# Kernel optimization log

Hardware: AMD Instinct MI355X
Metric: run time of the kernel (lower is better)

## Reference

```python
import jax, jax.numpy as jnp
import numpy as np

N, E, D_IN, D, HEADS = 8192, 2048, 256, 256, 4
EPS = 1e-5
NEG = -1e9  # large negative instead of -inf (rows guaranteed non-empty anyway)


def _layernorm(x, g, b):
    mu = jnp.mean(x, axis=-1, keepdims=True)
    var = jnp.mean(jnp.square(x - mu), axis=-1, keepdims=True)
    return (x - mu) * jax.lax.rsqrt(var + EPS) * g + b


def _mha(q_x, kv_x, in_w, in_b, out_w, out_b, mask):
    """torch nn.MultiheadAttention (batch=1, eval) with boolean attn_mask.
    q_x: [Lq, D], kv_x: [Lk, D], mask: [Lq, Lk] True = blocked."""
    hd = D // HEADS
    wq, wk, wv = jnp.split(in_w, 3, axis=0)   # each [D, D]
    bq, bk, bv = jnp.split(in_b, 3, axis=0)
    q = (q_x @ wq.T + bq).reshape(-1, HEADS, hd).transpose(1, 0, 2)  # [h, Lq, hd]
    k = (kv_x @ wk.T + bk).reshape(-1, HEADS, hd).transpose(1, 0, 2)
    v = (kv_x @ wv.T + bv).reshape(-1, HEADS, hd).transpose(1, 0, 2)
    scores = jnp.einsum('hqd,hkd->hqk', q, k) / jnp.sqrt(jnp.asarray(hd, q.dtype))
    scores = jnp.where(mask[None, :, :], NEG, scores)
    attn = jax.nn.softmax(scores, axis=-1)
    out = jnp.einsum('hqk,hkd->hqd', attn, v)           # [h, Lq, hd]
    out = out.transpose(1, 0, 2).reshape(-1, D)          # [Lq, D]
    return out @ out_w.T + out_b


def setup_inputs() -> dict:
    key = jax.random.key(0)
    ks = jax.random.split(key, 12)
    s = 0.02
    x_0 = jax.random.normal(ks[0], (N, D_IN), jnp.float32)
    x_1 = jax.random.normal(ks[1], (E, D_IN), jnp.float32)
    H = (jax.random.uniform(ks[2], (N, E)) < 0.01).astype(jnp.float32)
    H = H.at[jnp.arange(N), jnp.arange(N) % E].set(1.0)
    return {
        'x_0': x_0, 'x_1': x_1, 'incidence_1': H,
        'node_w': jax.random.normal(ks[3], (D, D_IN), jnp.float32) * s,
        'node_b': jnp.zeros((D,), jnp.float32),
        'edge_w': jax.random.normal(ks[4], (D, D_IN), jnp.float32) * s,
        'edge_b': jnp.zeros((D,), jnp.float32),
        'n2e_in_w': jax.random.normal(ks[5], (3 * D, D), jnp.float32) * s,
        'n2e_in_b': jnp.zeros((3 * D,), jnp.float32),
        'n2e_out_w': jax.random.normal(ks[6], (D, D), jnp.float32) * s,
        'n2e_out_b': jnp.zeros((D,), jnp.float32),
        'e2n_in_w': jax.random.normal(ks[7], (3 * D, D), jnp.float32) * s,
        'e2n_in_b': jnp.zeros((3 * D,), jnp.float32),
        'e2n_out_w': jax.random.normal(ks[8], (D, D), jnp.float32) * s,
        'e2n_out_b': jnp.zeros((D,), jnp.float32),
        'norm1_g': jnp.ones((D,), jnp.float32),
        'norm1_b': jnp.zeros((D,), jnp.float32),
        'norm2_g': jnp.ones((D,), jnp.float32),
        'norm2_b': jnp.zeros((D,), jnp.float32),
    }


def reference(x_0, x_1, incidence_1, node_w, node_b, edge_w, edge_b,
              n2e_in_w, n2e_in_b, n2e_out_w, n2e_out_b,
              e2n_in_w, e2n_in_b, e2n_out_w, e2n_out_b,
              norm1_g, norm1_b, norm2_g, norm2_b):
    H = incidence_1                      # [N, E]
    x_0_p = x_0 @ node_w.T + node_b      # [N, D]
    x_1_p = x_1 @ edge_w.T + edge_b      # [E, D]
    # node -> edge: edges query nodes, mask where H.T == 0
    x_1_u = _mha(x_1_p, x_0_p, n2e_in_w, n2e_in_b, n2e_out_w, n2e_out_b,
                 H.T == 0)
    x_1_u = _layernorm(x_1_p + x_1_u, norm1_g, norm1_b)
    # edge -> node: nodes query updated edges, mask where H == 0
    x_0_u = _mha(x_0_p, x_1_u, e2n_in_w, e2n_in_b, e2n_out_w, e2n_out_b,
                 H == 0)
    x_0_u = _layernorm(x_0_p + x_0_u, norm2_g, norm2_b)
    return (x_0_u, x_1_u)
```

## Files before the change

kernel.cpp:

```cpp
#include <hip/hip_runtime.h>
#include <hip/hip_bf16.h>

using bf16 = __hip_bfloat16;
typedef __attribute__((ext_vector_type(4))) float  f32x4;
typedef __attribute__((ext_vector_type(8))) short  s16x8;

#define QSTRIDE 1040
#define CMAX 256
#define RMAX 128

struct ConvDesc { const float* src[12]; int dstoff[12]; int cnt[12]; };

__global__ __launch_bounds__(256)
void conv_weights(ConvDesc d, bf16* __restrict__ dst)
{
    const int seg = blockIdx.x >> 6;
    const int blk = blockIdx.x & 63;
    const float* __restrict__ s = d.src[seg];
    bf16* __restrict__ o = dst + d.dstoff[seg];
    const int n = d.cnt[seg];
    for (int i = blk * 256 + threadIdx.x; i < n; i += 64 * 256)
        o[i] = __float2bfloat16(s[i]);
}

__global__ __launch_bounds__(256)
void build_lists(const float* __restrict__ H, int* __restrict__ col_cnt,
                 unsigned short* __restrict__ col_idx, int* __restrict__ row_cnt,
                 unsigned short* __restrict__ row_idx)
{
    const int n = blockIdx.x, t = threadIdx.x;
    __shared__ int rc;
    if (t == 0) rc = 0;
    __syncthreads();

    const float* Hp = H + (size_t)n * 2048 + t * 8;
    f32x4 h0 = *(const f32x4*)Hp;
    f32x4 h1 = *(const f32x4*)(Hp + 4);
    float hv[8];
#pragma unroll
    for (int j = 0; j < 4; j++) { hv[j] = h0[j]; hv[4 + j] = h1[j]; }

#pragma unroll
    for (int j = 0; j < 8; j++) {
        if (hv[j] != 0.f) {
            const int e = t * 8 + j;
            const int sr = atomicAdd(&rc, 1);
            if (sr < RMAX) row_idx[(size_t)n * RMAX + sr] = (unsigned short)e;
            const int sc = atomicAdd(&col_cnt[e], 1);
            if (sc < CMAX) col_idx[(size_t)e * CMAX + sc] = (unsigned short)n;
        }
    }
    __syncthreads();
    if (t == 0) row_cnt[n] = (rc < RMAX) ? rc : RMAX;
}

template<bool AF32>
__global__ __launch_bounds__(256, 2)
void gemm_bt(const void* __restrict__ Av, const bf16* __restrict__ W,
             const bf16* __restrict__ bias, bf16* __restrict__ outB,
             int K, int N, int tilesN)
{
    __shared__ __align__(16) bf16 As[4 * QSTRIDE];
    __shared__ __align__(16) bf16 Bs[4 * QSTRIDE];

    const int t    = threadIdx.x;
    const int lane = t & 63;
    const int w    = t >> 6;
    const int wm   = (w >> 1) * 64;
    const int wn   = (w & 1) * 64;
    const int tm   = (blockIdx.x / tilesN) * 128;
    const int tn   = (blockIdx.x % tilesN) * 128;

    f32x4 acc[4][4];
#pragma unroll
    for (int i = 0; i < 4; i++)
#pragma unroll
        for (int j = 0; j < 4; j++)
#pragma unroll
            for (int r = 0; r < 4; r++) acc[i][j][r] = 0.f;

    const int m0 = t >> 2,         q0 = t & 3;
    const int m1 = (t + 256) >> 2, q1 = (t + 256) & 3;

    const int fq = lane >> 4;
    const int fr = lane & 15;

    for (int k0 = 0; k0 < K; k0 += 32) {
        s16x8 sa0, sa1;
        if (AF32) {
            const float* Af = (const float*)Av;
            f32x4 a0l = *(const f32x4*)(Af + (size_t)(tm + m0) * K + k0 + q0 * 8);
            f32x4 a0h = *(const f32x4*)(Af + (size_t)(tm + m0) * K + k0 + q0 * 8 + 4);
            f32x4 a1l = *(const f32x4*)(Af + (size_t)(tm + m1) * K + k0 + q1 * 8);
            f32x4 a1h = *(const f32x4*)(Af + (size_t)(tm + m1) * K + k0 + q1 * 8 + 4);
            union { s16x8 v; bf16 e[8]; } u0, u1;
#pragma unroll
            for (int j = 0; j < 4; j++) {
                u0.e[j] = __float2bfloat16(a0l[j]); u0.e[4 + j] = __float2bfloat16(a0h[j]);
                u1.e[j] = __float2bfloat16(a1l[j]); u1.e[4 + j] = __float2bfloat16(a1h[j]);
            }
            sa0 = u0.v; sa1 = u1.v;
        } else {
            const bf16* Ab = (const bf16*)Av;
            sa0 = *(const s16x8*)(Ab + (size_t)(tm + m0) * K + k0 + q0 * 8);
            sa1 = *(const s16x8*)(Ab + (size_t)(tm + m1) * K + k0 + q1 * 8);
        }
        s16x8 sb0 = *(const s16x8*)(W + (size_t)(tn + m0) * K + k0 + q0 * 8);
        s16x8 sb1 = *(const s16x8*)(W + (size_t)(tn + m1) * K + k0 + q1 * 8);

        __syncthreads();
        *(s16x8*)&As[q0 * QSTRIDE + m0 * 8] = sa0;
        *(s16x8*)&As[q1 * QSTRIDE + m1 * 8] = sa1;
        *(s16x8*)&Bs[q0 * QSTRIDE + m0 * 8] = sb0;
        *(s16x8*)&Bs[q1 * QSTRIDE + m1 * 8] = sb1;
        __syncthreads();

        s16x8 af[4], bfv[4];
#pragma unroll
        for (int i = 0; i < 4; i++) {
            af[i]  = *(const s16x8*)&As[fq * QSTRIDE + (wm + i * 16 + fr) * 8];
            bfv[i] = *(const s16x8*)&Bs[fq * QSTRIDE + (wn + i * 16 + fr) * 8];
        }
#pragma unroll
        for (int i = 0; i < 4; i++)
#pragma unroll
            for (int j = 0; j < 4; j++)
                acc[i][j] = __builtin_amdgcn_mfma_f32_16x16x32_bf16(
                    af[i], bfv[j], acc[i][j], 0, 0, 0);
    }

#pragma unroll
    for (int j = 0; j < 4; j++) {
        const int ncol = tn + wn + j * 16 + fr;
        const float bj = __bfloat162float(bias[ncol]);
#pragma unroll
        for (int i = 0; i < 4; i++)
#pragma unroll
            for (int r = 0; r < 4; r++) {
                const int mrow = tm + wm + i * 16 + fq * 4 + r;
                outB[(size_t)mrow * N + ncol] = __float2bfloat16(acc[i][j][r] + bj);
            }
    }
}

__global__ __launch_bounds__(256)
void sparse_attn(const bf16* __restrict__ Q, const bf16* __restrict__ Kb,
                 const bf16* __restrict__ Vb, int kvs,
                 const int* __restrict__ cnts, const unsigned short* __restrict__ idx,
                 int lmax, int idxmask, bf16* __restrict__ out)
{
    __shared__ float sc[4][CMAX];
    __shared__ unsigned short nls[CMAX];
    const int qi   = blockIdx.x;
    const int h    = threadIdx.x >> 6;
    const int lane = threadIdx.x & 63;
    const int grp  = lane >> 3;
    const int sub  = lane & 7;

    int n = cnts[qi];
    if (n > lmax) n = lmax;

    if (h == 0)
        for (int i = lane; i < n; i += 64)
            nls[i] = (unsigned short)(((int)idx[(size_t)qi * lmax + i]) & idxmask);
    __syncthreads();

    if (n <= 0) {
        out[(size_t)qi * 256 + h * 64 + lane] = __float2bfloat16(0.f);
        return;
    }

    float qv[8];
    {
        union { f32x4 v; unsigned short u[8]; } qu;
        qu.v = *(const f32x4*)(Q + (size_t)qi * 256 + h * 64 + sub * 8);
#pragma unroll
        for (int j = 0; j < 8; j++)
            qv[j] = __uint_as_float(((unsigned)qu.u[j]) << 16) * 0.125f;
    }

    float mx = -1e30f;
#pragma unroll 2
    for (int base = 0; base < n; base += 8) {
        const int i = base + grp;
        float s = -1e30f;
        if (i < n) {
            const int nb = nls[i];
            union { f32x4 v; unsigned short u[8]; } ku;
            ku.v = *(const f32x4*)(Kb + (size_t)nb * kvs + h * 64 + sub * 8);
            float a = 0.f;
#pragma unroll
            for (int j = 0; j < 8; j++)
                a += __uint_as_float(((unsigned)ku.u[j]) << 16) * qv[j];
            a += __shfl_xor(a, 1);
            a += __shfl_xor(a, 2);
            a += __shfl_xor(a, 4);
            if (sub == 0) sc[h][i] = a;
            s = a;
        }
        mx = fmaxf(mx, s);
    }
#pragma unroll
    for (int o = 32; o > 0; o >>= 1) mx = fmaxf(mx, __shfl_xor(mx, o));

    float sum = 0.f;
    for (int base = 0; base < n; base += 64) {
        const int i = base + lane;
        if (i < n) {
            const float p = __expf(sc[h][i] - mx);
            sc[h][i] = p;
            sum += p;
        }
    }
#pragma unroll
    for (int o = 32; o > 0; o >>= 1) sum += __shfl_xor(sum, o);
    const float inv = 1.f / sum;

    float oa[8];
#pragma unroll
    for (int j = 0; j < 8; j++) oa[j] = 0.f;
#pragma unroll 2
    for (int base = 0; base < n; base += 8) {
        const int i = base + grp;
        if (i < n) {
            const float p = sc[h][i];
            const int nb = nls[i];
            union { f32x4 v; unsigned short u[8]; } vu;
            vu.v = *(const f32x4*)(Vb + (size_t)nb * kvs + h * 64 + sub * 8);
#pragma unroll
            for (int j = 0; j < 8; j++)
                oa[j] += p * __uint_as_float(((unsigned)vu.u[j]) << 16);
        }
    }
#pragma unroll
    for (int j = 0; j < 8; j++) {
        oa[j] += __shfl_xor(oa[j], 8);
        oa[j] += __shfl_xor(oa[j], 16);
        oa[j] += __shfl_xor(oa[j], 32);
    }
    if (grp == 0) {
        union { s16x8 v; bf16 e[8]; } ou;
#pragma unroll
        for (int j = 0; j < 8; j++) ou.e[j] = __float2bfloat16(oa[j] * inv);
        *(s16x8*)(out + (size_t)qi * 256 + h * 64 + sub * 8) = ou.v;
    }
}

__global__ __launch_bounds__(256)
void residual_ln(const bf16* __restrict__ xp, const bf16* __restrict__ mh,
                 const float* __restrict__ g, const float* __restrict__ b,
                 float* __restrict__ outF, bf16* __restrict__ outB)
{
    const int row = blockIdx.x, t = threadIdx.x;
    __shared__ float red1[4], red2[4];
    const float x = __bfloat162float(xp[(size_t)row * 256 + t])
                  + __bfloat162float(mh[(size_t)row * 256 + t]);

    float s = x;
#pragma unroll
    for (int o = 32; o > 0; o >>= 1) s += __shfl_xor(s, o);
    if ((t & 63) == 0) red1[t >> 6] = s;
    __syncthreads();
    const float mu = (red1[0] + red1[1] + red1[2] + red1[3]) * (1.f / 256.f);

    const float d = x - mu;
    float v = d * d;
#pragma unroll
    for (int o = 32; o > 0; o >>= 1) v += __shfl_xor(v, o);
    if ((t & 63) == 0) red2[t >> 6] = v;
    __syncthreads();
    const float var = (red2[0] + red2[1] + red2[2] + red2[3]) * (1.f / 256.f);

    const float y = d * rsqrtf(var + 1e-5f) * g[t] + b[t];
    outF[(size_t)row * 256 + t] = y;
    if (outB) outB[(size_t)row * 256 + t] = __float2bfloat16(y);
}

extern "C" void kernel_launch(void* const* d_in, const int* in_sizes, int n_in,
                              void* d_out, int out_size, void* d_ws, size_t ws_size,
                              hipStream_t stream)
{
    const int N = 8192, E = 2048;

    float* out0 = (float*)d_out;
    float* out1 = (float*)d_out + (size_t)N * 256;

    char* wp = (char*)d_ws;
    auto carve = [&](size_t bytes) { void* p = wp; wp += (bytes + 15) & ~size_t(15); return p; };

    bf16*  wcat    = (bf16*)          carve(657920 * 2);
    int*   col_cnt = (int*)           carve((size_t)E * 4);
    int*   row_cnt = (int*)           carve((size_t)N * 4);
    unsigned short* col_idx = (unsigned short*)carve((size_t)E * CMAX * 2);
    unsigned short* row_idx = (unsigned short*)carve((size_t)N * RMAX * 2);
    bf16*  x0p     = (bf16*)          carve((size_t)N * 256 * 2);
    bf16*  x1p     = (bf16*)          carve((size_t)E * 256 * 2);
    bf16*  x1u_b   = (bf16*)          carve((size_t)E * 256 * 2);
    bf16*  R1      = (bf16*)          carve((size_t)N * 512 * 2);
    bf16*  R2      = (bf16*)          carve((size_t)E * 256 * 3 * 2);

    bf16* kv1   = R1;
    bf16* q2    = R1;
    bf16* attn2 = R1 + (size_t)N * 256;
    bf16* mha2  = R1;
    bf16* q1    = R2;
    bf16* attn1 = R2 + (size_t)E * 256;
    bf16* mha1  = R2 + (size_t)E * 512;
    bf16* kv2   = R2;

    const int O_NW = 0, O_EW = 65536, O_AIW = 131072, O_AOW = 327680,
              O_BIW = 393216, O_BOW = 589824, O_NB = 655360, O_EB = 655616,
              O_AIB = 655872, O_AOB = 656640, O_BIB = 656896, O_BOB = 657664;

    ConvDesc cd;
    const int srcix[12] = {3, 5, 7, 9, 11, 13, 4, 6, 8, 10, 12, 14};
    const int offs [12] = {O_NW, O_EW, O_AIW, O_AOW, O_BIW, O_BOW,
                           O_NB, O_EB, O_AIB, O_AOB, O_BIB, O_BOB};
    const int cnts [12] = {65536, 65536, 196608, 65536, 196608, 65536,
                           256, 256, 768, 256, 768, 256};
    for (int i = 0; i < 12; i++) {
        cd.src[i] = (const float*)d_in[srcix[i]];
        cd.dstoff[i] = offs[i];
        cd.cnt[i] = cnts[i];
    }
    conv_weights<<<12 * 64, 256, 0, stream>>>(cd, wcat);

    hipMemsetAsync(col_cnt, 0, (size_t)E * 4, stream);
    build_lists<<<N, 256, 0, stream>>>((const float*)d_in[2], col_cnt, col_idx,
                                       row_cnt, row_idx);

    gemm_bt<true><<<(N/128)*2, 256, 0, stream>>>(d_in[0], wcat + O_NW,
                                                 wcat + O_NB, x0p, 256, 256, 2);
    gemm_bt<true><<<(E/128)*2, 256, 0, stream>>>(d_in[1], wcat + O_EW,
                                                 wcat + O_EB, x1p, 256, 256, 2);

    gemm_bt<false><<<(E/128)*2, 256, 0, stream>>>(x1p, wcat + O_AIW,
                                                  wcat + O_AIB, q1, 256, 256, 2);
    gemm_bt<false><<<(N/128)*4, 256, 0, stream>>>(x0p, wcat + O_AIW + 65536,
                                                  wcat + O_AIB + 256, kv1, 256, 512, 4);
    sparse_attn<<<E, 256, 0, stream>>>(q1, kv1, kv1 + 256, 512,
                                       col_cnt, col_idx, CMAX, N - 1, attn1);
    gemm_bt<false><<<(E/128)*2, 256, 0, stream>>>(attn1, wcat + O_AOW,
                                                  wcat + O_AOB, mha1, 256, 256, 2);
    residual_ln<<<E, 256, 0, stream>>>(x1p, mha1, (const float*)d_in[15],
                                       (const float*)d_in[16], out1, x1u_b);

    gemm_bt<false><<<(N/128)*2, 256, 0, stream>>>(x0p, wcat + O_BIW,
                                                  wcat + O_BIB, q2, 256, 256, 2);
    gemm_bt<false><<<(E/128)*4, 256, 0, stream>>>(x1u_b, wcat + O_BIW + 65536,
                                                  wcat + O_BIB + 256, kv2, 256, 512, 4);
    sparse_attn<<<N, 256, 0, stream>>>(q2, kv2, kv2 + 256, 512,
                                       row_cnt, row_idx, RMAX, E - 1, attn2);
    gemm_bt<false><<<(N/128)*2, 256, 0, stream>>>(attn2, wcat + O_BOW,
                                                  wcat + O_BOB, mha2, 256, 256, 2);
    residual_ln<<<N, 256, 0, stream>>>(x0p, mha2, (const float*)d_in[17],
                                       (const float*)d_in[18], out0, nullptr);
}
```

Measured before the change: 288.1 us.

## Merge projection GEMMs, batch KV/Q GEMMs, fuse out-proj with residual LayerNorm

The two input projections become one launch (gemm_proj), which handles both the node and edge fp32 inputs. The node-side K/V projection for attention 1 and the Q projection for attention 2 are merged into a single 768-wide GEMM. The separate residual_ln kernels are removed: a new gemm_ln computes the output projection over full 256-column rows, adds bias and residual, and applies LayerNorm in the epilogue using shared-memory row reductions. This cuts kernel launches and intermediate round-trips through global memory. In exchange, gemm_ln uses 64-row tiles (fewer blocks) and computes variance as E[x^2]-mu^2, which can be less precise.

```diff
diff --git a/kernel.cpp b/kernel.cpp
--- a/kernel.cpp
+++ b/kernel.cpp
@@ -6,10 +6,12 @@
 typedef __attribute__((ext_vector_type(8))) short  s16x8;
 
 #define QSTRIDE 1040
+#define ASTRIDE 520
+#define BSTRIDE 2064
 #define CMAX 256
 #define RMAX 128
 
-struct ConvDesc { const float* src[12]; int dstoff[12]; int cnt[12]; };
+struct ConvDesc { const float* src[14]; int dstoff[14]; int cnt[14]; };
 
 __global__ __launch_bounds__(256)
 void conv_weights(ConvDesc d, bf16* __restrict__ dst)
@@ -54,9 +56,8 @@
     if (t == 0) row_cnt[n] = (rc < RMAX) ? rc : RMAX;
 }
 
-template<bool AF32>
 __global__ __launch_bounds__(256, 2)
-void gemm_bt(const void* __restrict__ Av, const bf16* __restrict__ W,
+void gemm_bt(const bf16* __restrict__ A, const bf16* __restrict__ W,
              const bf16* __restrict__ bias, bf16* __restrict__ outB,
              int K, int N, int tilesN)
 {
@@ -81,30 +82,11 @@
 
     const int m0 = t >> 2,         q0 = t & 3;
     const int m1 = (t + 256) >> 2, q1 = (t + 256) & 3;
-
-    const int fq = lane >> 4;
-    const int fr = lane & 15;
+    const int fq = lane >> 4, fr = lane & 15;
 
     for (int k0 = 0; k0 < K; k0 += 32) {
-        s16x8 sa0, sa1;
-        if (AF32) {
-            const float* Af = (const float*)Av;
-            f32x4 a0l = *(const f32x4*)(Af + (size_t)(tm + m0) * K + k0 + q0 * 8);
-            f32x4 a0h = *(const f32x4*)(Af + (size_t)(tm + m0) * K + k0 + q0 * 8 + 4);
-            f32x4 a1l = *(const f32x4*)(Af + (size_t)(tm + m1) * K + k0 + q1 * 8);
-            f32x4 a1h = *(const f32x4*)(Af + (size_t)(tm + m1) * K + k0 + q1 * 8 + 4);
-            union { s16x8 v; bf16 e[8]; } u0, u1;
-#pragma unroll
-            for (int j = 0; j < 4; j++) {
-                u0.e[j] = __float2bfloat16(a0l[j]); u0.e[4 + j] = __float2bfloat16(a0h[j]);
-                u1.e[j] = __float2bfloat16(a1l[j]); u1.e[4 + j] = __float2bfloat16(a1h[j]);
-            }
-            sa0 = u0.v; sa1 = u1.v;
-        } else {
-            const bf16* Ab = (const bf16*)Av;
-            sa0 = *(const s16x8*)(Ab + (size_t)(tm + m0) * K + k0 + q0 * 8);
-            sa1 = *(const s16x8*)(Ab + (size_t)(tm + m1) * K + k0 + q1 * 8);
-        }
+        s16x8 sa0 = *(const s16x8*)(A + (size_t)(tm + m0) * K + k0 + q0 * 8);
+        s16x8 sa1 = *(const s16x8*)(A + (size_t)(tm + m1) * K + k0 + q1 * 8);
         s16x8 sb0 = *(const s16x8*)(W + (size_t)(tn + m0) * K + k0 + q0 * 8);
         s16x8 sb1 = *(const s16x8*)(W + (size_t)(tn + m1) * K + k0 + q1 * 8);
 
@@ -143,9 +125,205 @@
     }
 }
 
+__global__ __launch_bounds__(256, 2)
+void gemm_proj(const float* __restrict__ X0, const float* __restrict__ X1,
+               const bf16* __restrict__ Wc, const bf16* __restrict__ biasc,
+               bf16* __restrict__ outB)
+{
+    __shared__ __align__(16) bf16 As[4 * QSTRIDE];
+    __shared__ __align__(16) bf16 Bs[4 * QSTRIDE];
+
+    const int t    = threadIdx.x;
+    const int lane = t & 63;
+    const int w    = t >> 6;
+    const int wm   = (w >> 1) * 64;
+    const int wn   = (w & 1) * 64;
+    const int bt   = blockIdx.x >> 1;
+    const int tn   = (blockIdx.x & 1) * 128;
+    if (bt >= 80) return;
+
+    const float* __restrict__ A = (bt < 64) ? X0 : X1;
+    const int arow = (bt < 64) ? bt * 128 : (bt - 64) * 128;
+    const bf16* __restrict__ W    = Wc    + ((bt < 64) ? 0 : 65536);
+    const bf16* __restrict__ bias = biasc + ((bt < 64) ? 0 : 256);
+    const int tm = bt * 128;
+
+    f32x4 acc[4][4];
+#pragma unroll
+    for (int i = 0; i < 4; i++)
+#pragma unroll
+        for (int j = 0; j < 4; j++)
+#pragma unroll
+            for (int r = 0; r < 4; r++) acc[i][j][r] = 0.f;
+
+    const int m0 = t >> 2,         q0 = t & 3;
+    const int m1 = (t + 256) >> 2, q1 = (t + 256) & 3;
+    const int fq = lane >> 4, fr = lane & 15;
+
+    for (int k0 = 0; k0 < 256; k0 += 32) {
+        f32x4 a0l = *(const f32x4*)(A + (size_t)(arow + m0) * 256 + k0 + q0 * 8);
+        f32x4 a0h = *(const f32x4*)(A + (size_t)(arow + m0) * 256 + k0 + q0 * 8 + 4);
+        f32x4 a1l = *(const f32x4*)(A + (size_t)(arow + m1) * 256 + k0 + q1 * 8);
+        f32x4 a1h = *(const f32x4*)(A + (size_t)(arow + m1) * 256 + k0 + q1 * 8 + 4);
+        union { s16x8 v; bf16 e[8]; } u0, u1;
+#pragma unroll
+        for (int j = 0; j < 4; j++) {
+            u0.e[j] = __float2bfloat16(a0l[j]); u0.e[4 + j] = __float2bfloat16(a0h[j]);
+            u1.e[j] = __float2bfloat16(a1l[j]); u1.e[4 + j] = __float2bfloat16(a1h[j]);
+        }
+        s16x8 sb0 = *(const s16x8*)(W + (size_t)(tn + m0) * 256 + k0 + q0 * 8);
+        s16x8 sb1 = *(const s16x8*)(W + (size_t)(tn + m1) * 256 + k0 + q1 * 8);
+
+        __syncthreads();
+        *(s16x8*)&As[q0 * QSTRIDE + m0 * 8] = u0.v;
+        *(s16x8*)&As[q1 * QSTRIDE + m1 * 8] = u1.v;
+        *(s16x8*)&Bs[q0 * QSTRIDE + m0 * 8] = sb0;
+        *(s16x8*)&Bs[q1 * QSTRIDE + m1 * 8] = sb1;
+        __syncthreads();
+
+        s16x8 af[4], bfv[4];
+#pragma unroll
+        for (int i = 0; i < 4; i++) {
+            af[i]  = *(const s16x8*)&As[fq * QSTRIDE + (wm + i * 16 + fr) * 8];
+            bfv[i] = *(const s16x8*)&Bs[fq * QSTRIDE + (wn + i * 16 + fr) * 8];
+        }
+#pragma unroll
+        for (int i = 0; i < 4; i++)
+#pragma unroll
+            for (int j = 0; j < 4; j++)
+                acc[i][j] = __builtin_amdgcn_mfma_f32_16x16x32_bf16(
+                    af[i], bfv[j], acc[i][j], 0, 0, 0);
+    }
+
+#pragma unroll
+    for (int j = 0; j < 4; j++) {
+        const int ncol = tn + wn + j * 16 + fr;
+        const float bj = __bfloat162float(bias[ncol]);
+#pragma unroll
+        for (int i = 0; i < 4; i++)
+#pragma unroll
+            for (int r = 0; r < 4; r++) {
+                const int mrow = tm + wm + i * 16 + fq * 4 + r;
+                outB[(size_t)mrow * 256 + ncol] = __float2bfloat16(acc[i][j][r] + bj);
+            }
+    }
+}
+
+__global__ __launch_bounds__(256, 2)
+void gemm_ln(const bf16* __restrict__ A, const bf16* __restrict__ W,
+             const float* __restrict__ biasF, const bf16* __restrict__ xp,
+             const float* __restrict__ g, const float* __restrict__ b,
+             float* __restrict__ outF, bf16* __restrict__ outB)
+{
+    __shared__ __align__(16) bf16 As[4 * ASTRIDE];
+    __shared__ __align__(16) bf16 Bs[4 * BSTRIDE];
+    __shared__ float rs1[64], rs2[64];
+
+    const int t    = threadIdx.x;
+    const int lane = t & 63;
+    const int w    = t >> 6;
+    const int fq   = lane >> 4;
+    const int fr   = lane & 15;
+    const int tm   = blockIdx.x * 64;
+
+    if (t < 64) { rs1[t] = 0.f; rs2[t] = 0.f; }
+
+    f32x4 acc[4][4];
+#pragma unroll
+    for (int i = 0; i < 4; i++)
+#pragma unroll
+        for (int j = 0; j < 4; j++)
+#pragma unroll
+            for (int r = 0; r < 4; r++) acc[i][j][r] = 0.f;
+
+    const int mA = t >> 2, qA = t & 3;
+
+    for (int k0 = 0; k0 < 256; k0 += 32) {
+        s16x8 sa = *(const s16x8*)(A + (size_t)(tm + mA) * 256 + k0 + qA * 8);
+        s16x8 sb[4];
+#pragma unroll
+        for (int s = 0; s < 4; s++)
+            sb[s] = *(const s16x8*)(W + (size_t)(mA + 64 * s) * 256 + k0 + qA * 8);
+
+        __syncthreads();
+        *(s16x8*)&As[qA * ASTRIDE + mA * 8] = sa;
+#pragma unroll
+        for (int s = 0; s < 4; s++)
+            *(s16x8*)&Bs[qA * BSTRIDE + (mA + 64 * s) * 8] = sb[s];
+        __syncthreads();
+
+        s16x8 af[4], bfv[4];
+#pragma unroll
+        for (int i = 0; i < 4; i++) {
+            af[i]  = *(const s16x8*)&As[fq * ASTRIDE + (i * 16 + fr) * 8];
+            bfv[i] = *(const s16x8*)&Bs[fq * BSTRIDE + (w * 64 + i * 16 + fr) * 8];
+        }
+#pragma unroll
+        for (int i = 0; i < 4; i++)
+#pragma unroll
+            for (int j = 0; j < 4; j++)
+                acc[i][j] = __builtin_amdgcn_mfma_f32_16x16x32_bf16(
+                    af[i], bfv[j], acc[i][j], 0, 0, 0);
+    }
+
+    float bj[4], gj[4], bbj[4];
+    int colv[4];
+#pragma unroll
+    for (int j = 0; j < 4; j++) {
+        colv[j] = w * 64 + j * 16 + fr;
+        bj[j]  = biasF[colv[j]];
+        gj[j]  = g[colv[j]];
+        bbj[j] = b[colv[j]];
+    }
+
+#pragma unroll
+    for (int i = 0; i < 4; i++) {
+#pragma unroll
+        for (int r = 0; r < 4; r++) {
+            const int row = i * 16 + fq * 4 + r;
+            float t1 = 0.f, t2 = 0.f;
+#pragma unroll
+            for (int j = 0; j < 4; j++) {
+                float v = acc[i][j][r] + bj[j]
+                        + __bfloat162float(xp[(size_t)(tm + row) * 256 + colv[j]]);
+                acc[i][j][r] = v;
+                t1 += v;
+                t2 += v * v;
+            }
+#pragma unroll
+            for (int o = 1; o < 16; o <<= 1) {
+                t1 += __shfl_xor(t1, o);
+                t2 += __shfl_xor(t2, o);
+            }
+            if (fr == 0) {
+                atomicAdd(&rs1[row], t1);
+                atomicAdd(&rs2[row], t2);
+            }
+        }
+    }
+    __syncthreads();
+
+#pragma unroll
+    for (int i = 0; i < 4; i++) {
+#pragma unroll
+        for (int r = 0; r < 4; r++) {
+            const int row = i * 16 + fq * 4 + r;
+            const float mu  = rs1[row] * (1.f / 256.f);
+            const float var = rs2[row] * (1.f / 256.f) - mu * mu;
+            const float rstd = rsqrtf(var + 1e-5f);
+#pragma unroll
+            for (int j = 0; j < 4; j++) {
+                const float y = (acc[i][j][r] - mu) * rstd * gj[j] + bbj[j];
+                outF[(size_t)(tm + row) * 256 + colv[j]] = y;
+                if (outB) outB[(size_t)(tm + row) * 256 + colv[j]] = __float2bfloat16(y);
+            }
+        }
+    }
+}
+
 __global__ __launch_bounds__(256)
-void sparse_attn(const bf16* __restrict__ Q, const bf16* __restrict__ Kb,
-                 const bf16* __restrict__ Vb, int kvs,
+void sparse_attn(const bf16* __restrict__ Q, int qs,
+                 const bf16* __restrict__ Kb, const bf16* __restrict__ Vb, int kvs,
                  const int* __restrict__ cnts, const unsigned short* __restrict__ idx,
                  int lmax, int idxmask, bf16* __restrict__ out)
 {
@@ -173,7 +351,7 @@
     float qv[8];
     {
         union { f32x4 v; unsigned short u[8]; } qu;
-        qu.v = *(const f32x4*)(Q + (size_t)qi * 256 + h * 64 + sub * 8);
+        qu.v = *(const f32x4*)(Q + (size_t)qi * qs + h * 64 + sub * 8);
 #pragma unroll
         for (int j = 0; j < 8; j++)
             qv[j] = __uint_as_float(((unsigned)qu.u[j]) << 16) * 0.125f;
@@ -246,36 +424,6 @@
     }
 }
 
-__global__ __launch_bounds__(256)
-void residual_ln(const bf16* __restrict__ xp, const bf16* __restrict__ mh,
-                 const float* __restrict__ g, const float* __restrict__ b,
-                 float* __restrict__ outF, bf16* __restrict__ outB)
-{
-    const int row = blockIdx.x, t = threadIdx.x;
-    __shared__ float red1[4], red2[4];
-    const float x = __bfloat162float(xp[(size_t)row * 256 + t])
-                  + __bfloat162float(mh[(size_t)row * 256 + t]);
-
-    float s = x;
-#pragma unroll
-    for (int o = 32; o > 0; o >>= 1) s += __shfl_xor(s, o);
-    if ((t & 63) == 0) red1[t >> 6] = s;
-    __syncthreads();
-    const float mu = (red1[0] + red1[1] + red1[2] + red1[3]) * (1.f / 256.f);
-
-    const float d = x - mu;
-    float v = d * d;
-#pragma unroll
-    for (int o = 32; o > 0; o >>= 1) v += __shfl_xor(v, o);
-    if ((t & 63) == 0) red2[t >> 6] = v;
-    __syncthreads();
-    const float var = (red2[0] + red2[1] + red2[2] + red2[3]) * (1.f / 256.f);
-
-    const float y = d * rsqrtf(var + 1e-5f) * g[t] + b[t];
-    outF[(size_t)row * 256 + t] = y;
-    if (outB) outB[(size_t)row * 256 + t] = __float2bfloat16(y);
-}
-
 extern "C" void kernel_launch(void* const* d_in, const int* in_sizes, int n_in,
                               void* d_out, int out_size, void* d_ws, size_t ws_size,
                               hipStream_t stream)
@@ -288,71 +436,74 @@
     char* wp = (char*)d_ws;
     auto carve = [&](size_t bytes) { void* p = wp; wp += (bytes + 15) & ~size_t(15); return p; };
 
-    bf16*  wcat    = (bf16*)          carve(657920 * 2);
+    bf16*  wcat    = (bf16*)          carve(657408 * 2);
     int*   col_cnt = (int*)           carve((size_t)E * 4);
     int*   row_cnt = (int*)           carve((size_t)N * 4);
     unsigned short* col_idx = (unsigned short*)carve((size_t)E * CMAX * 2);
     unsigned short* row_idx = (unsigned short*)carve((size_t)N * RMAX * 2);
-    bf16*  x0p     = (bf16*)          carve((size_t)N * 256 * 2);
-    bf16*  x1p     = (bf16*)          carve((size_t)E * 256 * 2);
-    bf16*  x1u_b   = (bf16*)          carve((size_t)E * 256 * 2);
-    bf16*  R1      = (bf16*)          carve((size_t)N * 512 * 2);
-    bf16*  R2      = (bf16*)          carve((size_t)E * 256 * 3 * 2);
-
-    bf16* kv1   = R1;
-    bf16* q2    = R1;
-    bf16* attn2 = R1 + (size_t)N * 256;
-    bf16* mha2  = R1;
-    bf16* q1    = R2;
-    bf16* attn1 = R2 + (size_t)E * 256;
-    bf16* mha1  = R2 + (size_t)E * 512;
-    bf16* kv2   = R2;
-
-    const int O_NW = 0, O_EW = 65536, O_AIW = 131072, O_AOW = 327680,
-              O_BIW = 393216, O_BOW = 589824, O_NB = 655360, O_EB = 655616,
-              O_AIB = 655872, O_AOB = 656640, O_BIB = 656896, O_BOB = 657664;
+    bf16*  xp01    = (bf16*) carve((size_t)(N + E) * 256 * 2);
+    bf16*  kvq     = (bf16*) carve((size_t)N * 768 * 2);
+    bf16*  q1      = (bf16*) carve((size_t)E * 256 * 2);
+    bf16*  attn1   = (bf16*) carve((size_t)E * 256 * 2);
+    bf16*  x1u_b   = (bf16*) carve((size_t)E * 256 * 2);
+    bf16*  kv2     = (bf16*) carve((size_t)E * 512 * 2);
+    bf16*  attn2   = (bf16*) carve((size_t)N * 256 * 2);
+
+    bf16* x0p = xp01;
+    bf16* x1p = xp01 + (size_t)N * 256;
+
+    const int O_PW   = 0;
+    const int O_PB   = 131072;
+    const int O_KVQ  = 131584;
+    const int O_KVQB = 328192;
+    const int O_Q1W  = 328960;
+    const int O_Q1B  = 394496;
+    const int O_KV2W = 394752;
+    const int O_KV2B = 525824;
+    const int O_O1W  = 526336;
+    const int O_O2W  = 591872;
 
     ConvDesc cd;
-    const int srcix[12] = {3, 5, 7, 9, 11, 13, 4, 6, 8, 10, 12, 14};
-    const int offs [12] = {O_NW, O_EW, O_AIW, O_AOW, O_BIW, O_BOW,
-                           O_NB, O_EB, O_AIB, O_AOB, O_BIB, O_BOB};
-    const int cnts [12] = {65536, 65536, 196608, 65536, 196608, 65536,
-                           256, 256, 768, 256, 768, 256};
-    for (int i = 0; i < 12; i++) {
-        cd.src[i] = (const float*)d_in[srcix[i]];
-        cd.dstoff[i] = offs[i];
-        cd.cnt[i] = cnts[i];
-    }
-    conv_weights<<<12 * 64, 256, 0, stream>>>(cd, wcat);
+    const float* srcs[14] = {
+        (const float*)d_in[3], (const float*)d_in[5],
+        (const float*)d_in[4], (const float*)d_in[6],
+        (const float*)d_in[7] + 65536, (const float*)d_in[11],
+        (const float*)d_in[8] + 256,   (const float*)d_in[12],
+        (const float*)d_in[7],         (const float*)d_in[8],
+        (const float*)d_in[11] + 65536,(const float*)d_in[12] + 256,
+        (const float*)d_in[9],         (const float*)d_in[13]
+    };
+    const int offs[14] = {O_PW, O_PW + 65536, O_PB, O_PB + 256,
+                          O_KVQ, O_KVQ + 131072, O_KVQB, O_KVQB + 512,
+                          O_Q1W, O_Q1B, O_KV2W, O_KV2B, O_O1W, O_O2W};
+    const int cnts[14] = {65536, 65536, 256, 256, 131072, 65536, 512, 256,
+                          65536, 256, 131072, 512, 65536, 65536};
+    for (int i = 0; i < 14; i++) { cd.src[i] = srcs[i]; cd.dstoff[i] = offs[i]; cd.cnt[i] = cnts[i]; }
+    conv_weights<<<14 * 64, 256, 0, stream>>>(cd, wcat);
 
     hipMemsetAsync(col_cnt, 0, (size_t)E * 4, stream);
     build_lists<<<N, 256, 0, stream>>>((const float*)d_in[2], col_cnt, col_idx,
                                        row_cnt, row_idx);
 
-    gemm_bt<true><<<(N/128)*2, 256, 0, stream>>>(d_in[0], wcat + O_NW,
-                                                 wcat + O_NB, x0p, 256, 256, 2);
-    gemm_bt<true><<<(E/128)*2, 256, 0, stream>>>(d_in[1], wcat + O_EW,
-                                                 wcat + O_EB, x1p, 256, 256, 2);
-
-    gemm_bt<false><<<(E/128)*2, 256, 0, stream>>>(x1p, wcat + O_AIW,
-                                                  wcat + O_AIB, q1, 256, 256, 2);
-    gemm_bt<false><<<(N/128)*4, 256, 0, stream>>>(x0p, wcat + O_AIW + 65536,
-                                                  wcat + O_AIB + 256, kv1, 256, 512, 4);
-    sparse_attn<<<E, 256, 0, stream>>>(q1, kv1, kv1 + 256, 512,
+    gemm_proj<<<160, 256, 0, stream>>>((const float*)d_in[0], (const float*)d_in[1],
+                                       wcat + O_PW, wcat + O_PB, xp01);
+
+    gemm_bt<<<(N / 128) * 6, 256, 0, stream>>>(x0p, wcat + O_KVQ, wcat + O_KVQB,
+                                               kvq, 256, 768, 6);
+    gemm_bt<<<(E / 128) * 2, 256, 0, stream>>>(x1p, wcat + O_Q1W, wcat + O_Q1B,
+                                               q1, 256, 256, 2);
+
+    sparse_attn<<<E, 256, 0, stream>>>(q1, 256, kvq, kvq + 256, 768,
                                        col_cnt, col_idx, CMAX, N - 1, attn1);
-    gemm_bt<false><<<(E/128)*2, 256, 0, stream>>>(attn1, wcat + O_AOW,
-                                                  wcat + O_AOB, mha1, 256, 256, 2);
-    residual_ln<<<E, 256, 0, stream>>>(x1p, mha1, (const float*)d_in[15],
-                                       (const float*)d_in[16], out1, x1u_b);
-
-    gemm_bt<false><<<(N/128)*2, 256, 0, stream>>>(x0p, wcat + O_BIW,
-                                                  wcat + O_BIB, q2, 256, 256, 2);
-    gemm_bt<false><<<(E/128)*4, 256, 0, stream>>>(x1u_b, wcat + O_BIW + 65536,
-                                                  wcat + O_BIB + 256, kv2, 256, 512, 4);
-    sparse_attn<<<N, 256, 0, stream>>>(q2, kv2, kv2 + 256, 512,
+    gemm_ln<<<E / 64, 256, 0, stream>>>(attn1, wcat + O_O1W, (const float*)d_in[10],
+                                        x1p, (const float*)d_in[15], (const float*)d_in[16],
+                                        out1, x1u_b);
+
+    gemm_bt<<<(E / 128) * 4, 256, 0, stream>>>(x1u_b, wcat + O_KV2W, wcat + O_KV2B,
+                                               kv2, 256, 512, 4);
+    sparse_attn<<<N, 256, 0, stream>>>(kvq + 512, 768, kv2, kv2 + 256, 512,
                                        row_cnt, row_idx, RMAX, E - 1, attn2);
-    gemm_bt<false><<<(N/128)*2, 256, 0, stream>>>(attn2, wcat + O_BOW,
-                                                  wcat + O_BOB, mha2, 256, 256, 2);
-    residual_ln<<<N, 256, 0, stream>>>(x0p, mha2, (const float*)d_in[17],
-                                       (const float*)d_in[18], out0, nullptr);
-}
+    gemm_ln<<<N / 64, 256, 0, stream>>>(attn2, wcat + O_O2W, (const float*)d_in[14],
+                                        x0p, (const float*)d_in[17], (const float*)d_in[18],
+                                        out0, nullptr);
+}
```

New measurement: 273.7 us. 5.0% less time.
